# Kernel optimization log

Hardware: AMD Instinct MI355X
Metric: run time of the kernel (lower is better)

Reference implementation:

```python
import jax, jax.numpy as jnp
import numpy as np

B, C, H, W = 8, 128, 64, 64


def _conv1x1(t, w, b):
    # t: [B,C,H,W], w: [O,C], b: [O]  (torch Conv2d k=1 weight squeezed)
    return jnp.einsum('bchw,oc->bohw', t, w) + b[None, :, None, None]


def setup_inputs() -> dict:
    key = jax.random.key(0)
    ks = jax.random.split(key, 6)
    s = 1.0 / np.sqrt(C)  # conv init scale
    return {
        'x': jax.random.normal(ks[0], (B, C, H, W), dtype=jnp.float32),
        'freq_weights': jnp.ones((C,), dtype=jnp.float32),
        'wq': jax.random.normal(ks[1], (C, C), dtype=jnp.float32) * s,
        'bq': jnp.zeros((C,), dtype=jnp.float32),
        'wk': jax.random.normal(ks[2], (C, C), dtype=jnp.float32) * s,
        'bk': jnp.zeros((C,), dtype=jnp.float32),
        'wv': jax.random.normal(ks[3], (C, C), dtype=jnp.float32) * s,
        'bv': jnp.zeros((C,), dtype=jnp.float32),
        'wo': jax.random.normal(ks[4], (C, C), dtype=jnp.float32) * s,
        'bo': jnp.zeros((C,), dtype=jnp.float32),
    }


def reference(x, freq_weights, wq, bq, wk, bk, wv, bv, wo, bo):
    b, c, h, w = x.shape
    n = h * w
    # FFT-domain magnitude reweighting (faithful abs/angle reconstruction)
    fd = jnp.fft.fft2(x, axes=(-2, -1))
    mag = jnp.abs(fd)
    freq_attn = mag * freq_weights[None, :, None, None]
    refined_freq = freq_attn * jnp.exp(1j * jnp.angle(fd))
    refined = jnp.fft.ifft2(refined_freq, axes=(-2, -1)).real.astype(x.dtype)
    # 1x1-conv Q/K/V projections
    q = _conv1x1(refined, wq, bq).reshape(b, c, n)
    k = _conv1x1(refined, wk, bk).reshape(b, c, n)
    v = _conv1x1(refined, wv, bv).reshape(b, c, n)
    # Spatial self-attention over HW tokens, features = channels
    scores = jnp.einsum('bcn,bcm->bnm', q, k) / jnp.sqrt(jnp.asarray(c, x.dtype))
    attn = jax.nn.softmax(scores, axis=-1)  # [B, HW, HW]
    out = jnp.einsum('bnm,bcm->bcn', attn, v).reshape(b, c, h, w)
    return _conv1x1(out, wo, bo)
```

## Files before the change

### kernel.cpp

```cpp
#include <hip/hip_runtime.h>
#include <hip/hip_bf16.h>
#include <math.h>


typedef __bf16 bf16;
typedef _Float16 f16;
typedef __bf16 bf16x8 __attribute__((ext_vector_type(8)));
typedef __bf16 bf16x4 __attribute__((ext_vector_type(4)));
typedef __bf16 bf16x2 __attribute__((ext_vector_type(2)));
typedef _Float16 f16x8 __attribute__((ext_vector_type(8)));
typedef float  f32x4  __attribute__((ext_vector_type(4)));
typedef unsigned int u32x4 __attribute__((ext_vector_type(4)));

#define MFMA16(a, b, c) __builtin_amdgcn_mfma_f32_16x16x32_bf16((a), (b), (c), 0, 0, 0)

static constexpr int BATCH = 8;
static constexpr int CH    = 128;
static constexpr int NTOK  = 4096;
static constexpr int XS    = 136;
static constexpr int PS    = 72;
static constexpr int MS    = 136;
static constexpr float FIXM = 8.0f;

__device__ inline bf16x8 cvt8(const float* p, float s) {
  f32x4 a = *(const f32x4*)p;
  f32x4 b = *(const f32x4*)(p + 4);
  bf16x8 r;
  #pragma unroll
  for (int i = 0; i < 4; ++i) { r[i] = (bf16)(a[i] * s); r[4 + i] = (bf16)(b[i] * s); }
  return r;
}

__global__ __launch_bounds__(512) void proj_kernel(
    const float* __restrict__ x, const float* __restrict__ fw,
    const float* __restrict__ wq, const float* __restrict__ wk,
    const float* __restrict__ wv,
    const float* __restrict__ bq, const float* __restrict__ bk,
    const float* __restrict__ bv,
    bf16* __restrict__ Qt, bf16* __restrict__ Kt, bf16* __restrict__ Vt,
    float qscale)
{
  const int wg = blockIdx.x;
  const int b = wg >> 6, tile = wg & 63;
  const int t = threadIdx.x;
  const int w = t >> 6, lane = t & 63, quad = lane >> 4, l15 = lane & 15;

  __shared__ bf16 Xt[64 * XS];

  const float* xb = x + (size_t)b * CH * NTOK + tile * 64;
  #pragma unroll
  for (int i = 0; i < 8; ++i) {
    int c = (i * 8 + w) * 2;
    float f0 = fw[c], f1 = fw[c + 1];
    float x0 = xb[(size_t)c * NTOK + lane] * f0;
    float x1 = xb[(size_t)(c + 1) * NTOK + lane] * f1;
    bf16x2 pk; pk.x = (bf16)x0; pk.y = (bf16)x1;
    *(bf16x2*)(&Xt[lane * XS + c]) = pk;
  }
  __syncthreads();

  bf16x8 xfrag[4][4];
  #pragma unroll
  for (int st = 0; st < 4; ++st)
    #pragma unroll
    for (int ks = 0; ks < 4; ++ks)
      xfrag[st][ks] = *(const bf16x8*)(&Xt[(st * 16 + l15) * XS + ks * 32 + quad * 8]);

  const size_t wrow = (size_t)(w * 16 + l15) * CH;
  const int tokb = tile * 64;

  {
    bf16x8 qw[4];
    #pragma unroll
    for (int ks = 0; ks < 4; ++ks) qw[ks] = cvt8(wq + wrow + ks * 32 + quad * 8, qscale);
    f32x4 acc[4];
    #pragma unroll
    for (int st = 0; st < 4; ++st) acc[st] = (f32x4){0.f, 0.f, 0.f, 0.f};
    #pragma unroll
    for (int ks = 0; ks < 4; ++ks)
      #pragma unroll
      for (int st = 0; st < 4; ++st)
        acc[st] = MFMA16(qw[ks], xfrag[st][ks], acc[st]);
    float bias[4];
    #pragma unroll
    for (int r = 0; r < 4; ++r) bias[r] = bq[w * 16 + quad * 4 + r] * qscale;
    #pragma unroll
    for (int st = 0; st < 4; ++st) {
      bf16x4 o;
      #pragma unroll
      for (int r = 0; r < 4; ++r) o[r] = (bf16)(acc[st][r] + bias[r]);
      *(bf16x4*)(&Qt[(size_t)(b * NTOK + tokb + st * 16 + l15) * CH + w * 16 + quad * 4]) = o;
    }
  }
  {
    bf16x8 kw[4];
    #pragma unroll
    for (int ks = 0; ks < 4; ++ks) kw[ks] = cvt8(wk + wrow + ks * 32 + quad * 8, 1.0f);
    f32x4 acc[4];
    #pragma unroll
    for (int st = 0; st < 4; ++st) acc[st] = (f32x4){0.f, 0.f, 0.f, 0.f};
    #pragma unroll
    for (int ks = 0; ks < 4; ++ks)
      #pragma unroll
      for (int st = 0; st < 4; ++st)
        acc[st] = MFMA16(kw[ks], xfrag[st][ks], acc[st]);
    float bias[4];
    #pragma unroll
    for (int r = 0; r < 4; ++r) bias[r] = bk[w * 16 + quad * 4 + r];
    #pragma unroll
    for (int st = 0; st < 4; ++st) {
      bf16x4 o;
      #pragma unroll
      for (int r = 0; r < 4; ++r) o[r] = (bf16)(acc[st][r] + bias[r]);
      *(bf16x4*)(&Kt[(size_t)(b * NTOK + tokb + st * 16 + l15) * CH + w * 16 + quad * 4]) = o;
    }
  }
  {
    bf16x8 vw[4];
    #pragma unroll
    for (int ks = 0; ks < 4; ++ks) vw[ks] = cvt8(wv + wrow + ks * 32 + quad * 8, 1.0f);
    f32x4 acc[4];
    #pragma unroll
    for (int st = 0; st < 4; ++st) acc[st] = (f32x4){0.f, 0.f, 0.f, 0.f};
    #pragma unroll
    for (int ks = 0; ks < 4; ++ks)
      #pragma unroll
      for (int st = 0; st < 4; ++st)
        acc[st] = MFMA16(xfrag[st][ks], vw[ks], acc[st]);
    float bias = bv[w * 16 + l15];
    #pragma unroll
    for (int st = 0; st < 4; ++st) {
      bf16x4 o;
      #pragma unroll
      for (int r = 0; r < 4; ++r) o[r] = (bf16)(acc[st][r] + bias);
      *(bf16x4*)(&Vt[((size_t)b * CH + w * 16 + l15) * NTOK + tokb + st * 16 + quad * 4]) = o;
    }
  }
}

__global__ __launch_bounds__(256, 2) void flash_part_kernel(
    const bf16* __restrict__ Qt, const bf16* __restrict__ Kt,
    const bf16* __restrict__ Vt, f16* __restrict__ Op, float* __restrict__ Lp,
    int nslab, int ntile)
{
  const int wg = blockIdx.x;
  const int qt = wg & 31;
  const int slab = (wg >> 5) % nslab;
  const int b = wg / (nslab * 32);
  const int t = threadIdx.x;
  const int w = t >> 6, lane = t & 63, quad = lane >> 4, l15 = lane & 15;
  const int swz = l15 & 7;

  __shared__ bf16 ldsK[64 * 128];
  __shared__ bf16 ldsV[128 * 64];
  __shared__ bf16 ldsP[4 * 32 * PS];

  bf16x8 qfrag[2][4];
  #pragma unroll
  for (int s2 = 0; s2 < 2; ++s2) {
    const bf16* qb = Qt + ((size_t)b * NTOK + qt * 128 + w * 32 + s2 * 16 + l15) * CH;
    #pragma unroll
    for (int ks = 0; ks < 4; ++ks)
      qfrag[s2][ks] = *(const bf16x8*)(qb + ks * 32 + quad * 8);
  }

  f32x4 o_acc[2][8];
  #pragma unroll
  for (int s2 = 0; s2 < 2; ++s2)
    #pragma unroll
    for (int nt = 0; nt < 8; ++nt) o_acc[s2][nt] = (f32x4){0.f, 0.f, 0.f, 0.f};
  float lsum[2] = {0.f, 0.f};

  const bf16* kb = Kt + ((size_t)b * NTOK + slab * ntile * 64) * CH;
  const bf16* vb = Vt + (size_t)b * CH * NTOK + slab * ntile * 64;
  bf16* Pw = ldsP + w * 32 * PS;

  const bf16* kg[4]; bf16* kl[4];
  const bf16* vg[4]; bf16* vl[4];
  #pragma unroll
  for (int i = 0; i < 4; ++i) {
    int idx = t + i * 256;
    { int row = idx >> 4, cb = idx & 15;
      kg[i] = kb + (size_t)idx * 8;
      kl[i] = &ldsK[row * 128 + ((cb ^ (row & 7)) * 8)]; }
    { int row = idx >> 3, cb = idx & 7;
      vg[i] = vb + (size_t)row * NTOK + cb * 8;
      vl[i] = &ldsV[row * 64 + ((cb ^ (row & 7)) * 8)]; }
  }

  u32x4 rk[4], rv[4];
  #pragma unroll
  for (int i = 0; i < 4; ++i) {
    rk[i] = *(const u32x4*)kg[i];
    rv[i] = *(const u32x4*)vg[i];
    kg[i] += 64 * CH;
    vg[i] += 64;
  }

  for (int kt = 0; kt < ntile; ++kt) {
    __syncthreads();
    #pragma unroll
    for (int i = 0; i < 4; ++i) {
      *(u32x4*)kl[i] = rk[i];
      *(u32x4*)vl[i] = rv[i];
    }
    __syncthreads();

    if (kt < ntile - 1) {
      #pragma unroll
      for (int i = 0; i < 4; ++i) {
        rk[i] = *(const u32x4*)kg[i];
        rv[i] = *(const u32x4*)vg[i];
        kg[i] += 64 * CH;
        vg[i] += 64;
      }
    }

    #pragma unroll
    for (int mt = 0; mt < 4; ++mt) {
      f32x4 s[2];
      s[0] = (f32x4){0.f, 0.f, 0.f, 0.f};
      s[1] = (f32x4){0.f, 0.f, 0.f, 0.f};
      __builtin_amdgcn_s_setprio(1);
      #pragma unroll
      for (int ks = 0; ks < 4; ++ks) {
        bf16x8 kfr = *(const bf16x8*)(&ldsK[(mt * 16 + l15) * 128 + (((ks * 4 + quad) ^ swz) * 8)]);
        s[0] = MFMA16(kfr, qfrag[0][ks], s[0]);
        s[1] = MFMA16(kfr, qfrag[1][ks], s[1]);
      }
      __builtin_amdgcn_s_setprio(0);
      #pragma unroll
      for (int s2 = 0; s2 < 2; ++s2) {
        f32x4 v = s[s2];
        bf16x4 pk;
        float ps = 0.f;
        #pragma unroll
        for (int r = 0; r < 4; ++r) {
          float p = exp2f(v[r] - FIXM);
          ps += p;
          pk[r] = (bf16)p;
        }
        lsum[s2] += ps;
        *(bf16x4*)(&Pw[(s2 * 16 + l15) * PS + mt * 16 + quad * 4]) = pk;
      }
    }

    bf16x8 pfrag[2][2];
    #pragma unroll
    for (int s2 = 0; s2 < 2; ++s2)
      #pragma unroll
      for (int c = 0; c < 2; ++c)
        pfrag[s2][c] = *(const bf16x8*)(&Pw[(s2 * 16 + l15) * PS + c * 32 + quad * 8]);

    __builtin_amdgcn_s_setprio(1);
    #pragma unroll
    for (int k2 = 0; k2 < 2; ++k2)
      #pragma unroll
      for (int nt = 0; nt < 8; ++nt) {
        bf16x8 vfr = *(const bf16x8*)(&ldsV[(nt * 16 + l15) * 64 + (((k2 * 4 + quad) ^ swz) * 8)]);
        o_acc[0][nt] = MFMA16(pfrag[0][k2], vfr, o_acc[0][nt]);
        o_acc[1][nt] = MFMA16(pfrag[1][k2], vfr, o_acc[1][nt]);
      }
    __builtin_amdgcn_s_setprio(0);
  }

  const size_t obase = ((size_t)(slab * BATCH + b) * NTOK + qt * 128 + w * 32) * CH;
  #pragma unroll
  for (int s2 = 0; s2 < 2; ++s2)
    #pragma unroll
    for (int nt = 0; nt < 8; ++nt)
      #pragma unroll
      for (int r = 0; r < 4; ++r) {
        int row = s2 * 16 + quad * 4 + r;
        Op[obase + (size_t)row * CH + nt * 16 + l15] = (f16)o_acc[s2][nt][r];
      }
  #pragma unroll
  for (int s2 = 0; s2 < 2; ++s2) {
    float v = lsum[s2];
    v += __shfl_xor(v, 16);
    v += __shfl_xor(v, 32);
    if (quad == 0)
      Lp[(size_t)(slab * BATCH + b) * NTOK + qt * 128 + w * 32 + s2 * 16 + l15] = v;
  }
}

__global__ __launch_bounds__(256) void merge_kernel(
    const f16* __restrict__ Op, const float* __restrict__ Lp,
    const float* __restrict__ wo, const float* __restrict__ bo,
    float* __restrict__ out, int nslab)
{
  const int wg = blockIdx.x;
  const int b = wg >> 6, tile = wg & 63;
  const int t = threadIdx.x;
  const int w = t >> 6, lane = t & 63, quad = lane >> 4, l15 = lane & 15;

  __shared__ bf16 ldsO[64 * MS];

  const size_t slabO = (size_t)BATCH * NTOK * CH;
  const size_t slabL = (size_t)BATCH * NTOK;
  const f16* ob = Op + ((size_t)b * NTOK + tile * 64) * CH;
  const float* lp = Lp + (size_t)b * NTOK + tile * 64;

  #pragma unroll
  for (int i = 0; i < 4; ++i) {
    int idx = t + i * 256;
    int row = idx >> 4, cb = idx & 15;
    float lsum_ = 0.f;
    for (int s = 0; s < nslab; ++s) lsum_ += lp[s * slabL + row];
    float acc8[8] = {0.f, 0.f, 0.f, 0.f, 0.f, 0.f, 0.f, 0.f};
    for (int s = 0; s < nslab; ++s) {
      f16x8 a = *(const f16x8*)(ob + s * slabO + (size_t)row * CH + cb * 8);
      #pragma unroll
      for (int j = 0; j < 8; ++j) acc8[j] += (float)a[j];
    }
    float inv = 1.0f / lsum_;
    bf16 tmp[8];
    #pragma unroll
    for (int j = 0; j < 8; ++j) tmp[j] = (bf16)(acc8[j] * inv);
    *(u32x4*)(&ldsO[row * MS + cb * 8]) = *(u32x4*)tmp;
  }
  __syncthreads();

  #pragma unroll
  for (int mi = 0; mi < 2; ++mi) {
    int mt = w * 2 + mi;
    f32x4 facc[4];
    #pragma unroll
    for (int nt = 0; nt < 4; ++nt) facc[nt] = (f32x4){0.f, 0.f, 0.f, 0.f};
    #pragma unroll
    for (int ks = 0; ks < 4; ++ks) {
      bf16x8 afr = cvt8(wo + (size_t)(mt * 16 + l15) * CH + ks * 32 + quad * 8, 1.0f);
      #pragma unroll
      for (int nt = 0; nt < 4; ++nt) {
        bf16x8 bfr = *(const bf16x8*)(&ldsO[(nt * 16 + l15) * MS + ks * 32 + quad * 8]);
        facc[nt] = MFMA16(afr, bfr, facc[nt]);
      }
    }
    #pragma unroll
    for (int nt = 0; nt < 4; ++nt) {
      int n = tile * 64 + nt * 16 + l15;
      #pragma unroll
      for (int r = 0; r < 4; ++r) {
        int o = mt * 16 + quad * 4 + r;
        out[((size_t)b * CH + o) * NTOK + n] = facc[nt][r] + bo[o];
      }
    }
  }
}

extern "C" void kernel_launch(void* const* d_in, const int* in_sizes, int n_in,
                              void* d_out, int out_size, void* d_ws, size_t ws_size,
                              hipStream_t stream)
{
  const float* x  = (const float*)d_in[0];
  const float* fw = (const float*)d_in[1];
  const float* wq = (const float*)d_in[2];
  const float* bq = (const float*)d_in[3];
  const float* wk = (const float*)d_in[4];
  const float* bk = (const float*)d_in[5];
  const float* wv = (const float*)d_in[6];
  const float* bv = (const float*)d_in[7];
  const float* wo = (const float*)d_in[8];
  const float* bo = (const float*)d_in[9];
  float* out = (float*)d_out;

  char* ws = (char*)d_ws;
  bf16*  Qt  = (bf16*)ws;
  bf16*  Kt  = Qt + (size_t)BATCH * NTOK * CH;
  bf16*  Vt  = Kt + (size_t)BATCH * NTOK * CH;
  f16*   Op  = (f16*)(ws + 3ull * 8388608);

  const size_t qkv_bytes = 3ull * 8388608;
  const size_t need4 = qkv_bytes + 4ull * ((size_t)BATCH * NTOK * CH * 2 + (size_t)BATCH * NTOK * 4);
  const int S = (ws_size >= need4) ? 4 : 2;
  const int ntile = 64 / S;

  float* Lp = (float*)((char*)Op + (size_t)S * BATCH * NTOK * CH * 2);

  const float qscale = 0.08838834764831845f * 1.44269504f;

  proj_kernel<<<512, 512, 0, stream>>>(x, fw, wq, wk, wv,
                                       bq, bk, bv, Qt, Kt, Vt, qscale);
  flash_part_kernel<<<BATCH * S * 32, 256, 0, stream>>>(Qt, Kt, Vt, Op, Lp,
                                                        S, ntile);
  merge_kernel<<<512, 256, 0, stream>>>(Op, Lp, wo, bo, out, S);
}
```

Baseline: 208.2 us.

## Use three uneven KV slabs and halve the LDS P buffer via register stash

The KV split-count drops from 4 to 3 slabs, with uneven tile counts (base plus remainder) per slab. That gives 768 workgroups instead of 1024 and reduces partial-output traffic in the merge. The P staging buffer in LDS is halved: the second 16-row half of P is kept in registers and written into the same LDS area after the first half's fragments are read. This lowers LDS use and may allow higher occupancy, at the cost of extra LDS round-trips and more register pressure.

```diff
diff --git a/kernel.cpp b/kernel.cpp
--- a/kernel.cpp
+++ b/kernel.cpp
@@ -141,19 +141,21 @@
 __global__ __launch_bounds__(256, 2) void flash_part_kernel(
     const bf16* __restrict__ Qt, const bf16* __restrict__ Kt,
     const bf16* __restrict__ Vt, f16* __restrict__ Op, float* __restrict__ Lp,
-    int nslab, int ntile)
+    int nslab, int base, int rem)
 {
   const int wg = blockIdx.x;
   const int qt = wg & 31;
   const int slab = (wg >> 5) % nslab;
   const int b = wg / (nslab * 32);
+  const int ntile = base + (slab < rem ? 1 : 0);
+  const int koff  = slab * base + (slab < rem ? slab : rem);
   const int t = threadIdx.x;
   const int w = t >> 6, lane = t & 63, quad = lane >> 4, l15 = lane & 15;
   const int swz = l15 & 7;
 
   __shared__ bf16 ldsK[64 * 128];
   __shared__ bf16 ldsV[128 * 64];
-  __shared__ bf16 ldsP[4 * 32 * PS];
+  __shared__ bf16 ldsP[4 * 16 * PS];
 
   bf16x8 qfrag[2][4];
   #pragma unroll
@@ -171,9 +173,9 @@
     for (int nt = 0; nt < 8; ++nt) o_acc[s2][nt] = (f32x4){0.f, 0.f, 0.f, 0.f};
   float lsum[2] = {0.f, 0.f};
 
-  const bf16* kb = Kt + ((size_t)b * NTOK + slab * ntile * 64) * CH;
-  const bf16* vb = Vt + (size_t)b * CH * NTOK + slab * ntile * 64;
-  bf16* Pw = ldsP + w * 32 * PS;
+  const bf16* kb = Kt + ((size_t)b * NTOK + koff * 64) * CH;
+  const bf16* vb = Vt + (size_t)b * CH * NTOK + koff * 64;
+  bf16* Pw = ldsP + w * 16 * PS;
 
   const bf16* kg[4]; bf16* kl[4];
   const bf16* vg[4]; bf16* vl[4];
@@ -216,6 +218,7 @@
       }
     }
 
+    bf16x4 stash[4];
     #pragma unroll
     for (int mt = 0; mt < 4; ++mt) {
       f32x4 s[2];
@@ -241,16 +244,23 @@
           pk[r] = (bf16)p;
         }
         lsum[s2] += ps;
-        *(bf16x4*)(&Pw[(s2 * 16 + l15) * PS + mt * 16 + quad * 4]) = pk;
+        if (s2 == 0)
+          *(bf16x4*)(&Pw[l15 * PS + mt * 16 + quad * 4]) = pk;
+        else
+          stash[mt] = pk;
       }
     }
 
     bf16x8 pfrag[2][2];
     #pragma unroll
-    for (int s2 = 0; s2 < 2; ++s2)
-      #pragma unroll
-      for (int c = 0; c < 2; ++c)
-        pfrag[s2][c] = *(const bf16x8*)(&Pw[(s2 * 16 + l15) * PS + c * 32 + quad * 8]);
+    for (int c = 0; c < 2; ++c)
+      pfrag[0][c] = *(const bf16x8*)(&Pw[l15 * PS + c * 32 + quad * 8]);
+    #pragma unroll
+    for (int mt = 0; mt < 4; ++mt)
+      *(bf16x4*)(&Pw[l15 * PS + mt * 16 + quad * 4]) = stash[mt];
+    #pragma unroll
+    for (int c = 0; c < 2; ++c)
+      pfrag[1][c] = *(const bf16x8*)(&Pw[l15 * PS + c * 32 + quad * 8]);
 
     __builtin_amdgcn_s_setprio(1);
     #pragma unroll
@@ -371,9 +381,9 @@
   f16*   Op  = (f16*)(ws + 3ull * 8388608);
 
   const size_t qkv_bytes = 3ull * 8388608;
-  const size_t need4 = qkv_bytes + 4ull * ((size_t)BATCH * NTOK * CH * 2 + (size_t)BATCH * NTOK * 4);
-  const int S = (ws_size >= need4) ? 4 : 2;
-  const int ntile = 64 / S;
+  const size_t need3 = qkv_bytes + 3ull * ((size_t)BATCH * NTOK * CH * 2 + (size_t)BATCH * NTOK * 4);
+  const int S = (ws_size >= need3) ? 3 : 2;
+  const int base = 64 / S, rem = 64 % S;
 
   float* Lp = (float*)((char*)Op + (size_t)S * BATCH * NTOK * CH * 2);
 
@@ -382,6 +392,6 @@
   proj_kernel<<<512, 512, 0, stream>>>(x, fw, wq, wk, wv,
                                        bq, bk, bv, Qt, Kt, Vt, qscale);
   flash_part_kernel<<<BATCH * S * 32, 256, 0, stream>>>(Qt, Kt, Vt, Op, Lp,
-                                                        S, ntile);
+                                                        S, base, rem);
   merge_kernel<<<512, 256, 0, stream>>>(Op, Lp, wo, bo, out, S);
 }
```

New measurement: 212.1 us. Within noise of the previous version (+1.9%).
